# Optimization experiments

Hardware: AMD Instinct MI355X
Metric: run time of the kernel (lower is better)

Reference implementation:

```python
import jax, jax.numpy as jnp
import numpy as np

B, N, F_IN = 8, 1024, 64
HEADS = 8
D = F_IN  # out_features per head (in_features == out_features)


def setup_inputs() -> dict:
    key = jax.random.key(0)
    ks = jax.random.split(key, 5)
    stdv = 1.0 / np.sqrt(F_IN * HEADS)
    h = jax.random.normal(ks[0], (B, N, F_IN), dtype=jnp.float32)
    adj = jnp.ones((B, N, N), dtype=jnp.float32)  # passed but unused by the module
    W = jax.random.uniform(ks[1], (F_IN, D * HEADS), minval=-stdv, maxval=stdv, dtype=jnp.float32)
    a = jax.random.uniform(ks[2], (2 * D, 1), minval=-stdv, maxval=stdv, dtype=jnp.float32)
    out_W = jax.random.normal(ks[3], (D * HEADS, F_IN), dtype=jnp.float32) / np.sqrt(D * HEADS)
    out_b = jnp.zeros((F_IN,), dtype=jnp.float32)
    return {"h": h, "adj": adj, "W": W, "a": a, "out_W": out_W, "out_b": out_b}


def reference(h, adj, W, a, out_W, out_b):
    Bv, Nv, _ = h.shape
    Dh = W.shape[1] // HEADS
    # Wh: [B, N, H, D]
    Wh = (h @ W).reshape(Bv, Nv, HEADS, Dh)
    # Additive attention decomposed: e[b,i,j,h] = leaky_relu(Wh[b,i,h].a_src + Wh[b,j,h].a_dst)
    a_src = jnp.einsum('bnhd,d->bnh', Wh, a[:Dh, 0])
    a_dst = jnp.einsum('bnhd,d->bnh', Wh, a[Dh:, 0])
    e = jax.nn.leaky_relu(a_src[:, :, None, :] + a_dst[:, None, :, :], negative_slope=0.01)  # [B,N,N,H]
    # Module applies softmax over dim=1 (the first node axis i)
    attn = jax.nn.softmax(e, axis=1)  # [B,N,N,H]
    # h_prime[b,i,h,:] = sum_j attn[b,i,j,h] * Wh[b,j,h,:]
    h_prime = jnp.einsum('bijh,bjhd->bihd', attn, Wh).reshape(Bv, Nv, HEADS * Dh)
    return h_prime @ out_W + out_b
```

## Files before the change

kernel.cpp:

```cpp
#include <hip/hip_runtime.h>


#define B_  8
#define N_  1024
#define H_  8
#define D_  64
#define BH_ 64
#define CH_ 32
#define CL_ 32

__global__ __launch_bounds__(256) void k_wh(
    const float* __restrict__ h, const float* __restrict__ W,
    const float* __restrict__ a,
    float* __restrict__ Wh, float* __restrict__ sArr, float* __restrict__ tArr) {
  __shared__ float hL[16 * 64];
  __shared__ float whL[16 * 512];
  __shared__ float aL[128];
  const int tid = threadIdx.x;
  const int row0 = blockIdx.x * 16;
  const int b = row0 >> 10;
  for (int i = tid; i < 16 * 64; i += 256) hL[i] = h[row0 * 64 + i];
  if (tid < 128) aL[tid] = a[tid];
  __syncthreads();

  float acc0[16], acc1[16];
#pragma unroll
  for (int r = 0; r < 16; ++r) { acc0[r] = 0.f; acc1[r] = 0.f; }
  for (int k = 0; k < 64; ++k) {
    const float w0 = W[k * 512 + tid];
    const float w1 = W[k * 512 + tid + 256];
#pragma unroll
    for (int r = 0; r < 16; ++r) {
      const float hv = hL[r * 64 + k];
      acc0[r] += hv * w0;
      acc1[r] += hv * w1;
    }
  }
  const int hh0 = tid >> 6, d0 = tid & 63;
  const int hh1 = (tid + 256) >> 6;
#pragma unroll
  for (int r = 0; r < 16; ++r) {
    const int n = (row0 + r) & (N_ - 1);
    whL[r * 512 + tid] = acc0[r];
    whL[r * 512 + tid + 256] = acc1[r];
    Wh[((b * H_ + hh0) * N_ + n) * D_ + d0] = acc0[r];
    Wh[((b * H_ + hh1) * N_ + n) * D_ + d0] = acc1[r];
  }
  __syncthreads();
  if (tid < 128) {
    const int r = tid >> 3, hh = tid & 7;
    const int n = (row0 + r) & (N_ - 1);
    float accS = 0.f, accT = 0.f;
    for (int jj = 0; jj < 64; ++jj) {
      const int d = (jj + tid) & 63;
      const float wv = whL[r * 512 + hh * 64 + d];
      accS += wv * aL[d];
      accT += wv * aL[64 + d];
    }
    sArr[(b * H_ + hh) * N_ + n] = accS;
    tArr[(b * H_ + hh) * N_ + n] = accT;
  }
}

__global__ __launch_bounds__(1024) void k_sort(
    const float* __restrict__ sArr, const float* __restrict__ tArr,
    const float* __restrict__ Wh,
    int* __restrict__ tsi, float* __restrict__ uArr, float* __restrict__ vArr,
    int* __restrict__ qrk,
    float* __restrict__ cOff1, float* __restrict__ cOff2) {
  __shared__ float sL[1024];
  __shared__ float tvL[1024];
  __shared__ int   tiL[1024];
  __shared__ float cum1L[1024], cum001L[1024];
  __shared__ float uL[1024], vL[1024];
  __shared__ float cs1[CH_ * 64], cs2[CH_ * 64];
  __shared__ float ws1[16], ws2[16];
  const int tid = threadIdx.x;
  const int lane = tid & 63;
  const int wv_ = tid >> 6;
  const int bh = blockIdx.x;

  const float orig_s = sArr[bh * N_ + tid];
  float sv_r = orig_s;
  float tv_r = tArr[bh * N_ + tid];
  int   ti_r = tid;

  for (int size = 2; size <= 1024; size <<= 1) {
    for (int stride = size >> 1; stride > 0; stride >>= 1) {
      const bool up = ((tid & size) == 0);
      const bool lower = ((tid & stride) == 0);
      float psv, ptv; int pti;
      if (stride >= 64) {
        sL[tid] = sv_r; tvL[tid] = tv_r; tiL[tid] = ti_r;
        __syncthreads();
        const int p = tid ^ stride;
        psv = sL[p]; ptv = tvL[p]; pti = tiL[p];
        __syncthreads();
      } else {
        psv = __shfl_xor(sv_r, stride);
        ptv = __shfl_xor(tv_r, stride);
        pti = __shfl_xor(ti_r, stride);
      }
      const bool sameDir = (up == lower);
      const bool pLessS = (psv < sv_r);
      if (pLessS == sameDir) sv_r = psv;
      const bool pLessT = (ptv < tv_r) || (ptv == tv_r && pti < ti_r);
      if (pLessT == sameDir) { tv_r = ptv; ti_r = pti; }
    }
  }
  sL[tid] = sv_r; tvL[tid] = tv_r; tiL[tid] = ti_r;

  float c1 = __expf(sv_r) , c001 = __expf(0.01f * sv_r);
  {
    float a1 = c1, a2 = c001;
#pragma unroll
    for (int off = 1; off < 64; off <<= 1) {
      const float x1 = __shfl_up(a1, off);
      const float x2 = __shfl_up(a2, off);
      if (lane >= off) { a1 += x1; a2 += x2; }
    }
    if (lane == 63) { ws1[wv_] = a1; ws2[wv_] = a2; }
    __syncthreads();
    float o1 = 0.f, o2 = 0.f;
    for (int ww = 0; ww < 16; ++ww) {
      if (ww < wv_) { o1 += ws1[ww]; o2 += ws2[ww]; }
    }
    c1 = a1 + o1; c001 = a2 + o2;
  }
  cum1L[tid] = c1; cum001L[tid] = c001;
  __syncthreads();
  const float totalHi = cum1L[1023];

  {
    const float tj = tv_r;
    const float th = -tj;
    int lo = 0, hi = 1024;
    while (lo < hi) { const int mid = (lo + hi) >> 1; if (sL[mid] <= th) lo = mid + 1; else hi = mid; }
    const float S_lo = (lo > 0) ? cum001L[lo - 1] : 0.f;
    const float S_hi = totalHi - ((lo > 0) ? cum1L[lo - 1] : 0.f);
    const float et = __expf(tj), et001 = __expf(0.01f * tj);
    const float Z = et * S_hi + et001 * S_lo;
    const float u = et / Z, v = et001 / Z;
    uL[tid] = u; vL[tid] = v;
    uArr[bh * N_ + tid] = u; vArr[bh * N_ + tid] = v;
    tsi[bh * N_ + tid] = ti_r;
  }

  {
    const float th = -orig_s;
    int lo = 0, hi = 1024;
    while (lo < hi) { const int mid = (lo + hi) >> 1; if (tvL[mid] <= th) lo = mid + 1; else hi = mid; }
    qrk[bh * N_ + tid] = lo;
  }
  __syncthreads();

  const int c = tid >> 6, d = tid & 63;
#pragma unroll
  for (int half = 0; half < 2; ++half) {
    const int cc = c + half * 16;
    float s1 = 0.f, s2 = 0.f;
    for (int k2 = 0; k2 < CL_; ++k2) {
      const int k = cc * CL_ + k2;
      const int j = tiL[k];
      const float w = Wh[(bh * N_ + j) * D_ + d];
      s1 += uL[k] * w;
      s2 += vL[k] * w;
    }
    cs1[cc * 64 + d] = s1; cs2[cc * 64 + d] = s2;
  }
  __syncthreads();
#pragma unroll
  for (int half = 0; half < 2; ++half) {
    const int cc = c + half * 16;
    float o1 = 0.f, o2 = 0.f;
    for (int m = 0; m < cc; ++m) { o1 += cs1[m * 64 + d]; o2 += cs2[m * 64 + d]; }
    cOff1[(bh * CH_ + cc) * 64 + d] = o1;
    cOff2[(bh * CH_ + cc) * 64 + d] = o2;
  }
}

__global__ __launch_bounds__(64) void k_inc(
    const float* __restrict__ Wh, const int* __restrict__ tsi,
    const float* __restrict__ uArr, const float* __restrict__ vArr,
    const float* __restrict__ cOff1, const float* __restrict__ cOff2,
    float* __restrict__ INC1, float* __restrict__ INC2) {
  const int blk = blockIdx.x;
  const int bh = blk >> 5, c = blk & (CH_ - 1);
  const int d = threadIdx.x;
  float r1 = cOff1[blk * 64 + d];
  float r2 = cOff2[blk * 64 + d];
  const int base = bh * N_;
#pragma unroll 8
  for (int k2 = 0; k2 < CL_; ++k2) {
    const int k = c * CL_ + k2;
    const int j = tsi[base + k];
    const float u = uArr[base + k], v = vArr[base + k];
    const float w = Wh[(base + j) * D_ + d];
    r1 += u * w;
    r2 += v * w;
    INC1[(base + k) * D_ + d] = r1;
    INC2[(base + k) * D_ + d] = r2;
  }
}

__global__ __launch_bounds__(512) void k_out(
    const float* __restrict__ sArr, const int* __restrict__ qrk,
    const float* __restrict__ INC1, const float* __restrict__ INC2,
    const float* __restrict__ outW, const float* __restrict__ outb,
    float* __restrict__ out) {
  __shared__ float hpL[16 * 512];
  __shared__ float part[8 * 8 * 64];
  __shared__ int   rkI[16 * 8];
  __shared__ float esL[16 * 8], es001L[16 * 8];
  const int tid = threadIdx.x;
  const int row0 = blockIdx.x * 16;
  const int b = row0 >> 10;

  if (tid < 128) {
    const int r = tid >> 3, hh = tid & 7;
    const int bh = b * H_ + hh;
    const int n = (row0 + r) & (N_ - 1);
    const float si = sArr[bh * N_ + n];
    rkI[tid] = qrk[bh * N_ + n];
    esL[tid] = __expf(si);
    es001L[tid] = __expf(0.01f * si);
  }
  __syncthreads();

  {
    const int hh = tid >> 6, d = tid & 63;
    const int bh = b * H_ + hh;
    const float T1 = INC1[(bh * N_ + (N_ - 1)) * D_ + d];
    for (int r = 0; r < 16; ++r) {
      const int rk = rkI[r * 8 + hh];
      float i1 = 0.f, i2 = 0.f;
      if (rk > 0) {
        i1 = INC1[(bh * N_ + rk - 1) * D_ + d];
        i2 = INC2[(bh * N_ + rk - 1) * D_ + d];
      }
      hpL[r * 512 + hh * 64 + d] =
          esL[r * 8 + hh] * (T1 - i1) + es001L[r * 8 + hh] * i2;
    }
  }
  __syncthreads();

  const int cc = tid & 63, p = tid >> 6;
  float acc[16];
#pragma unroll
  for (int r = 0; r < 16; ++r) acc[r] = 0.f;
  for (int k = p * 64; k < p * 64 + 64; ++k) {
    const float wvv = outW[k * 64 + cc];
#pragma unroll
    for (int r = 0; r < 16; ++r) acc[r] += hpL[r * 512 + k] * wvv;
  }
  for (int half = 0; half < 2; ++half) {
#pragma unroll
    for (int r = 0; r < 8; ++r) part[(p * 8 + r) * 64 + cc] = acc[half * 8 + r];
    __syncthreads();
    {
      const int r = tid >> 6, c2 = tid & 63;
      float ssum = 0.f;
#pragma unroll
      for (int p2 = 0; p2 < 8; ++p2) ssum += part[(p2 * 8 + r) * 64 + c2];
      out[(row0 + half * 8 + r) * 64 + c2] = outb[c2] + ssum;
    }
    __syncthreads();
  }
}

extern "C" void kernel_launch(void* const* d_in, const int* in_sizes, int n_in,
                              void* d_out, int out_size, void* d_ws, size_t ws_size,
                              hipStream_t stream) {
  const float* h    = (const float*)d_in[0];
  const float* W    = (const float*)d_in[2];
  const float* a    = (const float*)d_in[3];
  const float* outW = (const float*)d_in[4];
  const float* outb = (const float*)d_in[5];
  float* out = (float*)d_out;

  float* ws   = (float*)d_ws;
  float* Wh   = ws;
  float* sArr = Wh + (size_t)BH_ * N_ * D_;
  float* tArr = sArr + BH_ * N_;
  int*   tsi  = (int*)(tArr + BH_ * N_);
  float* uArr = (float*)(tsi + BH_ * N_);
  float* vArr = uArr + BH_ * N_;
  int*   qrk  = (int*)(vArr + BH_ * N_);
  float* cOff1 = (float*)(qrk + BH_ * N_);
  float* cOff2 = cOff1 + BH_ * CH_ * 64;
  float* INC1 = cOff2 + BH_ * CH_ * 64;
  float* INC2 = INC1 + (size_t)BH_ * N_ * D_;

  hipLaunchKernelGGL(k_wh,   dim3((B_ * N_) / 16), dim3(256), 0, stream,
                     h, W, a, Wh, sArr, tArr);
  hipLaunchKernelGGL(k_sort, dim3(BH_), dim3(1024), 0, stream,
                     sArr, tArr, Wh, tsi, uArr, vArr, qrk, cOff1, cOff2);
  hipLaunchKernelGGL(k_inc,  dim3(BH_ * CH_), dim3(64), 0, stream,
                     Wh, tsi, uArr, vArr, cOff1, cOff2, INC1, INC2);
  hipLaunchKernelGGL(k_out,  dim3((B_ * N_) / 16), dim3(512), 0, stream,
                     sArr, qrk, INC1, INC2, outW, outb, out);
}
```

Before: 155.4 us.

## Fuse prefix-sum kernel into sort kernel and scatter h_prime per rank bucket

Merges the chunked prefix-sum kernel into the per-(batch,head) sort kernel. Instead of materialising full INC1/INC2 prefix arrays (64×1024×64 floats each), each block buckets query rows by rank using shared-memory counting sort. It then writes h_prime directly while walking its chunk of the sorted prefix sum. The output kernel then only loads h_prime and does the projection. This removes a launch and large global prefix-array traffic, but leaves only 64 blocks doing the serial prefix walk, with scattered 256-byte writes and shared atomics.

```diff
diff --git a/kernel.cpp b/kernel.cpp
--- a/kernel.cpp
+++ b/kernel.cpp
@@ -6,8 +6,8 @@
 #define H_  8
 #define D_  64
 #define BH_ 64
-#define CH_ 32
-#define CL_ 32
+#define NCH 16
+#define CLN 64
 
 __global__ __launch_bounds__(256) void k_wh(
     const float* __restrict__ h, const float* __restrict__ W,
@@ -62,28 +62,28 @@
   }
 }
 
-__global__ __launch_bounds__(1024) void k_sort(
+__global__ __launch_bounds__(1024) void k_mid(
     const float* __restrict__ sArr, const float* __restrict__ tArr,
-    const float* __restrict__ Wh,
-    int* __restrict__ tsi, float* __restrict__ uArr, float* __restrict__ vArr,
-    int* __restrict__ qrk,
-    float* __restrict__ cOff1, float* __restrict__ cOff2) {
-  __shared__ float sL[1024];
-  __shared__ float tvL[1024];
+    const float* __restrict__ Wh, float* __restrict__ hp) {
+  __shared__ float sL[1024], tvL[1024];
   __shared__ int   tiL[1024];
   __shared__ float cum1L[1024], cum001L[1024];
   __shared__ float uL[1024], vL[1024];
-  __shared__ float cs1[CH_ * 64], cs2[CH_ * 64];
-  __shared__ float ws1[16], ws2[16];
-  const int tid = threadIdx.x;
-  const int lane = tid & 63;
-  const int wv_ = tid >> 6;
+  __shared__ float esQ[1024], es001Q[1024];
+  __shared__ int   cntL[1025], startL[1025], qList[1024];
+  __shared__ float cs1[NCH * 64], cs2[NCH * 64];
+  __shared__ float wf1[16], wf2[16];
+  __shared__ int   wi1[16];
+  const int tid = threadIdx.x, lane = tid & 63, wv = tid >> 6;
   const int bh = blockIdx.x;
+  const int b = bh >> 3, hh = bh & 7;
 
   const float orig_s = sArr[bh * N_ + tid];
   float sv_r = orig_s;
   float tv_r = tArr[bh * N_ + tid];
   int   ti_r = tid;
+  cntL[tid] = 0;
+  if (tid == 0) cntL[1024] = 0;
 
   for (int size = 2; size <= 1024; size <<= 1) {
     for (int stride = size >> 1; stride > 0; stride >>= 1) {
@@ -91,11 +91,10 @@
       const bool lower = ((tid & stride) == 0);
       float psv, ptv; int pti;
       if (stride >= 64) {
+        __syncthreads();
         sL[tid] = sv_r; tvL[tid] = tv_r; tiL[tid] = ti_r;
         __syncthreads();
-        const int p = tid ^ stride;
-        psv = sL[p]; ptv = tvL[p]; pti = tiL[p];
-        __syncthreads();
+        psv = sL[tid ^ stride]; ptv = tvL[tid ^ stride]; pti = tiL[tid ^ stride];
       } else {
         psv = __shfl_xor(sv_r, stride);
         ptv = __shfl_xor(tv_r, stride);
@@ -110,20 +109,20 @@
   }
   sL[tid] = sv_r; tvL[tid] = tv_r; tiL[tid] = ti_r;
 
-  float c1 = __expf(sv_r) , c001 = __expf(0.01f * sv_r);
-  {
-    float a1 = c1, a2 = c001;
+  float c1, c001;
+  {
+    float a1 = __expf(sv_r), a2 = __expf(0.01f * sv_r);
 #pragma unroll
     for (int off = 1; off < 64; off <<= 1) {
       const float x1 = __shfl_up(a1, off);
       const float x2 = __shfl_up(a2, off);
       if (lane >= off) { a1 += x1; a2 += x2; }
     }
-    if (lane == 63) { ws1[wv_] = a1; ws2[wv_] = a2; }
+    if (lane == 63) { wf1[wv] = a1; wf2[wv] = a2; }
     __syncthreads();
     float o1 = 0.f, o2 = 0.f;
     for (int ww = 0; ww < 16; ++ww) {
-      if (ww < wv_) { o1 += ws1[ww]; o2 += ws2[ww]; }
+      if (ww < wv) { o1 += wf1[ww]; o2 += wf2[ww]; }
     }
     c1 = a1 + o1; c001 = a2 + o2;
   }
@@ -140,108 +139,99 @@
     const float S_hi = totalHi - ((lo > 0) ? cum1L[lo - 1] : 0.f);
     const float et = __expf(tj), et001 = __expf(0.01f * tj);
     const float Z = et * S_hi + et001 * S_lo;
-    const float u = et / Z, v = et001 / Z;
-    uL[tid] = u; vL[tid] = v;
-    uArr[bh * N_ + tid] = u; vArr[bh * N_ + tid] = v;
-    tsi[bh * N_ + tid] = ti_r;
-  }
-
+    uL[tid] = et / Z; vL[tid] = et001 / Z;
+  }
+
+  int rk;
   {
     const float th = -orig_s;
     int lo = 0, hi = 1024;
     while (lo < hi) { const int mid = (lo + hi) >> 1; if (tvL[mid] <= th) lo = mid + 1; else hi = mid; }
-    qrk[bh * N_ + tid] = lo;
-  }
-  __syncthreads();
-
-  const int c = tid >> 6, d = tid & 63;
-#pragma unroll
-  for (int half = 0; half < 2; ++half) {
-    const int cc = c + half * 16;
+    rk = lo;
+    atomicAdd(&cntL[rk], 1);
+    esQ[tid] = __expf(orig_s);
+    es001Q[tid] = __expf(0.01f * orig_s);
+  }
+  __syncthreads();
+
+  {
+    const int cown = cntL[tid];
+    int a = cown;
+#pragma unroll
+    for (int off = 1; off < 64; off <<= 1) {
+      const int x = __shfl_up(a, off);
+      if (lane >= off) a += x;
+    }
+    if (lane == 63) wi1[wv] = a;
+    __syncthreads();
+    int o = 0;
+    for (int ww = 0; ww < 16; ++ww) {
+      if (ww < wv) o += wi1[ww];
+    }
+    const int incl = a + o;
+    startL[tid] = incl - cown;
+    if (tid == 1023) startL[1024] = incl;
+  }
+  __syncthreads();
+  cntL[tid] = 0;
+  if (tid == 0) cntL[1024] = 0;
+  __syncthreads();
+  {
+    const int pos = startL[rk] + atomicAdd(&cntL[rk], 1);
+    qList[pos] = tid;
+  }
+
+  {
     float s1 = 0.f, s2 = 0.f;
-    for (int k2 = 0; k2 < CL_; ++k2) {
-      const int k = cc * CL_ + k2;
+    for (int k2 = 0; k2 < CLN; ++k2) {
+      const int k = wv * CLN + k2;
       const int j = tiL[k];
-      const float w = Wh[(bh * N_ + j) * D_ + d];
+      const float w = Wh[(bh * N_ + j) * D_ + lane];
       s1 += uL[k] * w;
       s2 += vL[k] * w;
     }
-    cs1[cc * 64 + d] = s1; cs2[cc * 64 + d] = s2;
-  }
-  __syncthreads();
-#pragma unroll
-  for (int half = 0; half < 2; ++half) {
-    const int cc = c + half * 16;
-    float o1 = 0.f, o2 = 0.f;
-    for (int m = 0; m < cc; ++m) { o1 += cs1[m * 64 + d]; o2 += cs2[m * 64 + d]; }
-    cOff1[(bh * CH_ + cc) * 64 + d] = o1;
-    cOff2[(bh * CH_ + cc) * 64 + d] = o2;
-  }
-}
-
-__global__ __launch_bounds__(64) void k_inc(
-    const float* __restrict__ Wh, const int* __restrict__ tsi,
-    const float* __restrict__ uArr, const float* __restrict__ vArr,
-    const float* __restrict__ cOff1, const float* __restrict__ cOff2,
-    float* __restrict__ INC1, float* __restrict__ INC2) {
-  const int blk = blockIdx.x;
-  const int bh = blk >> 5, c = blk & (CH_ - 1);
-  const int d = threadIdx.x;
-  float r1 = cOff1[blk * 64 + d];
-  float r2 = cOff2[blk * 64 + d];
-  const int base = bh * N_;
-#pragma unroll 8
-  for (int k2 = 0; k2 < CL_; ++k2) {
-    const int k = c * CL_ + k2;
-    const int j = tsi[base + k];
-    const float u = uArr[base + k], v = vArr[base + k];
-    const float w = Wh[(base + j) * D_ + d];
-    r1 += u * w;
-    r2 += v * w;
-    INC1[(base + k) * D_ + d] = r1;
-    INC2[(base + k) * D_ + d] = r2;
+    cs1[wv * 64 + lane] = s1; cs2[wv * 64 + lane] = s2;
+  }
+  __syncthreads();
+
+  float r1 = 0.f, r2 = 0.f, T1 = 0.f;
+  for (int m = 0; m < NCH; ++m) {
+    const float v1 = cs1[m * 64 + lane];
+    if (m < wv) { r1 += v1; r2 += cs2[m * 64 + lane]; }
+    T1 += v1;
+  }
+  for (int k2 = 0; k2 < CLN; ++k2) {
+    const int K = wv * CLN + k2;
+    const int qs = startL[K], qe = startL[K + 1];
+    for (int q = qs; q < qe; ++q) {
+      const int i = qList[q];
+      hp[((b * N_ + i) << 9) + (hh << 6) + lane] =
+          esQ[i] * (T1 - r1) + es001Q[i] * r2;
+    }
+    const int j = tiL[K];
+    const float w = Wh[(bh * N_ + j) * D_ + lane];
+    r1 += uL[K] * w;
+    r2 += vL[K] * w;
+  }
+  if (wv == NCH - 1) {
+    const int qs = startL[1024];
+    for (int q = qs; q < 1024; ++q) {
+      const int i = qList[q];
+      hp[((b * N_ + i) << 9) + (hh << 6) + lane] =
+          esQ[i] * (T1 - r1) + es001Q[i] * r2;
+    }
   }
 }
 
 __global__ __launch_bounds__(512) void k_out(
-    const float* __restrict__ sArr, const int* __restrict__ qrk,
-    const float* __restrict__ INC1, const float* __restrict__ INC2,
+    const float* __restrict__ hp,
     const float* __restrict__ outW, const float* __restrict__ outb,
     float* __restrict__ out) {
   __shared__ float hpL[16 * 512];
   __shared__ float part[8 * 8 * 64];
-  __shared__ int   rkI[16 * 8];
-  __shared__ float esL[16 * 8], es001L[16 * 8];
   const int tid = threadIdx.x;
   const int row0 = blockIdx.x * 16;
-  const int b = row0 >> 10;
-
-  if (tid < 128) {
-    const int r = tid >> 3, hh = tid & 7;
-    const int bh = b * H_ + hh;
-    const int n = (row0 + r) & (N_ - 1);
-    const float si = sArr[bh * N_ + n];
-    rkI[tid] = qrk[bh * N_ + n];
-    esL[tid] = __expf(si);
-    es001L[tid] = __expf(0.01f * si);
-  }
-  __syncthreads();
-
-  {
-    const int hh = tid >> 6, d = tid & 63;
-    const int bh = b * H_ + hh;
-    const float T1 = INC1[(bh * N_ + (N_ - 1)) * D_ + d];
-    for (int r = 0; r < 16; ++r) {
-      const int rk = rkI[r * 8 + hh];
-      float i1 = 0.f, i2 = 0.f;
-      if (rk > 0) {
-        i1 = INC1[(bh * N_ + rk - 1) * D_ + d];
-        i2 = INC2[(bh * N_ + rk - 1) * D_ + d];
-      }
-      hpL[r * 512 + hh * 64 + d] =
-          esL[r * 8 + hh] * (T1 - i1) + es001L[r * 8 + hh] * i2;
-    }
-  }
+  for (int i = tid; i < 16 * 512; i += 512) hpL[i] = hp[row0 * 512 + i];
   __syncthreads();
 
   const int cc = tid & 63, p = tid >> 6;
@@ -282,21 +272,12 @@
   float* Wh   = ws;
   float* sArr = Wh + (size_t)BH_ * N_ * D_;
   float* tArr = sArr + BH_ * N_;
-  int*   tsi  = (int*)(tArr + BH_ * N_);
-  float* uArr = (float*)(tsi + BH_ * N_);
-  float* vArr = uArr + BH_ * N_;
-  int*   qrk  = (int*)(vArr + BH_ * N_);
-  float* cOff1 = (float*)(qrk + BH_ * N_);
-  float* cOff2 = cOff1 + BH_ * CH_ * 64;
-  float* INC1 = cOff2 + BH_ * CH_ * 64;
-  float* INC2 = INC1 + (size_t)BH_ * N_ * D_;
-
-  hipLaunchKernelGGL(k_wh,   dim3((B_ * N_) / 16), dim3(256), 0, stream,
+  float* hpG  = tArr + BH_ * N_;
+
+  hipLaunchKernelGGL(k_wh,  dim3((B_ * N_) / 16), dim3(256), 0, stream,
                      h, W, a, Wh, sArr, tArr);
-  hipLaunchKernelGGL(k_sort, dim3(BH_), dim3(1024), 0, stream,
-                     sArr, tArr, Wh, tsi, uArr, vArr, qrk, cOff1, cOff2);
-  hipLaunchKernelGGL(k_inc,  dim3(BH_ * CH_), dim3(64), 0, stream,
-                     Wh, tsi, uArr, vArr, cOff1, cOff2, INC1, INC2);
-  hipLaunchKernelGGL(k_out,  dim3((B_ * N_) / 16), dim3(512), 0, stream,
-                     sArr, qrk, INC1, INC2, outW, outb, out);
-}
+  hipLaunchKernelGGL(k_mid, dim3(BH_), dim3(1024), 0, stream,
+                     sArr, tArr, Wh, hpG);
+  hipLaunchKernelGGL(k_out, dim3((B_ * N_) / 16), dim3(512), 0, stream,
+                     hpG, outW, outb, out);
+}
```

New measurement: 167.8 us. +7.9%, slower.
